# Optimization experiments

Measured on AMD Instinct MI355X. Metric: run time of the kernel, lower is better.

Reference implementation:

```python
import jax, jax.numpy as jnp
import numpy as np

B, T, D_MODEL = 2, 1024, 1024
H, DEPTH = 8, 5
DH = D_MODEL // H


def setup_inputs() -> dict:
    key = jax.random.key(0)
    k_x, k_wp, k_bp, k_wv, k_wo = jax.random.split(key, 5)
    x = jax.random.normal(k_x, (B, T, D_MODEL), dtype=jnp.float32)
    # Parameters stored as [in, out] (y = x @ W + b), equivalent math to nn.Linear.
    Wp = jax.random.normal(k_wp, (D_MODEL, H * DEPTH), dtype=jnp.float32) * 0.02
    bp = jnp.zeros((H * DEPTH,), dtype=jnp.float32)
    Wv = jax.random.normal(k_wv, (D_MODEL, D_MODEL), dtype=jnp.float32) * 0.02
    Wo = jax.random.normal(k_wo, (D_MODEL, D_MODEL), dtype=jnp.float32) * 0.02
    return {"x": x, "Wp": Wp, "bp": bp, "Wv": Wv, "Wo": Wo}


def reference(x, Wp, bp, Wv, Wo):
    Bx, Tx, d = x.shape
    # soft binary path decisions: B,H,T,DEPTH
    paths = jax.nn.sigmoid(x @ Wp + bp)              # B,T,H*DEPTH
    paths = paths.reshape(Bx, Tx, H, DEPTH).transpose(0, 2, 1, 3)  # B,H,T,DEPTH
    # pairwise per-level agreement: B,H,Tq,Tk,DEPTH
    pq = paths[:, :, :, None, :]
    pk = paths[:, :, None, :, :]
    agree = pq * pk + (1.0 - pq) * (1.0 - pk)
    # shared-prefix length via cumprod over depth, summed
    sim = jnp.cumprod(agree, axis=-1).sum(axis=-1) / DEPTH  # B,H,Tq,Tk
    # causal mask
    mask = jnp.triu(jnp.ones((Tx, Tx), dtype=bool), k=1)
    sim = jnp.where(mask[None, None], -jnp.inf, sim)
    attn = jax.nn.softmax(sim, axis=-1)              # B,H,T,T
    V = (x @ Wv).reshape(Bx, Tx, H, DH).transpose(0, 2, 1, 3)  # B,H,T,dh
    ctx = jnp.einsum('bhqk,bhkd->bhqd', attn, V)
    ctx = ctx.transpose(0, 2, 1, 3).reshape(Bx, Tx, d)
    return ctx @ Wo
```

## Files before the change

### kernel.cpp

```cpp
#include <hip/hip_runtime.h>
#include <hip/hip_bf16.h>

#define B_ 2
#define T_ 1024
#define D_ 1024
#define H_ 8
#define DEPTH_ 5
#define DH_ 128

typedef short s16x8 __attribute__((ext_vector_type(8)));
typedef short s16x4 __attribute__((ext_vector_type(4)));
typedef float f32x4 __attribute__((ext_vector_type(4)));

__device__ inline short f2bf(float f) {
  __hip_bfloat16 h = __float2bfloat16(f);
  return *reinterpret_cast<short*>(&h);
}

#define MFMA16(a, b, c) __builtin_amdgcn_mfma_f32_16x16x32_bf16(a, b, c, 0, 0, 0)

typedef __attribute__((address_space(3))) unsigned int lds_u32_t;
typedef __attribute__((address_space(1))) unsigned int glb_u32_t;
__device__ __forceinline__ void glds16(const void* g, void* l) {
  __builtin_amdgcn_global_load_lds((const glb_u32_t*)g, (lds_u32_t*)l, 16, 0,
                                   0);
}

__global__ __launch_bounds__(256) void prep_kernel(
    const float* __restrict__ Wv, const float* __restrict__ Wo,
    const float* __restrict__ Wp, const float* __restrict__ x,
    short* __restrict__ WBt, short* __restrict__ Wot,
    short* __restrict__ xb) {
  int tid = threadIdx.x;
  if (blockIdx.z < 2) {
    const float* W = blockIdx.z ? Wo : Wv;
    short* Wt = blockIdx.z ? Wot : WBt;
    __shared__ float tile[64][65];
    int k0 = blockIdx.y * 64, n0 = blockIdx.x * 64;
#pragma unroll
    for (int i = 0; i < 4; ++i) {
      int idx = tid + i * 256;
      int r = idx >> 4, c4 = (idx & 15) * 4;
      float4 v = *(const float4*)&W[(size_t)(k0 + r) * D_ + n0 + c4];
      tile[r][c4 + 0] = v.x;
      tile[r][c4 + 1] = v.y;
      tile[r][c4 + 2] = v.z;
      tile[r][c4 + 3] = v.w;
    }
    __syncthreads();
#pragma unroll
    for (int j = 0; j < 2; ++j) {
      int idx = tid + j * 256;
      int n = idx >> 3, k8 = (idx & 7) * 8;
      s16x8 outv;
#pragma unroll
      for (int jj = 0; jj < 8; ++jj) outv[jj] = f2bf(tile[k8 + jj][n]);
      *(s16x8*)&Wt[(size_t)(n0 + n) * D_ + k0 + k8] = outv;
    }
  } else {
    int bid = blockIdx.y * 16 + blockIdx.x;
#pragma unroll
    for (int c = 0; c < 4; ++c) {
      size_t idx = (size_t)bid * 8192 + c * 2048 + tid * 8;
      float4 f0 = *(const float4*)&x[idx];
      float4 f1 = *(const float4*)&x[idx + 4];
      s16x8 v;
      v[0] = f2bf(f0.x); v[1] = f2bf(f0.y);
      v[2] = f2bf(f0.z); v[3] = f2bf(f0.w);
      v[4] = f2bf(f1.x); v[5] = f2bf(f1.y);
      v[6] = f2bf(f1.z); v[7] = f2bf(f1.w);
      *(s16x8*)&xb[idx] = v;
    }
    if (bid < 4) {
#pragma unroll
      for (int it = 0; it < 8; ++it) {
        int item = bid * 2048 + it * 256 + tid;
        int row = item >> 7, k8 = (item & 127) * 8;
        s16x8 v;
        if (row < H_ * DEPTH_) {
#pragma unroll
          for (int j = 0; j < 8; ++j)
            v[j] = f2bf(Wp[(size_t)(k8 + j) * (H_ * DEPTH_) + row]);
        } else {
#pragma unroll
          for (int j = 0; j < 8; ++j) v[j] = 0;
        }
        *(s16x8*)&WBt[(size_t)(1024 + row) * D_ + k8] = v;
      }
    }
  }
}

template <int MODE>
__global__ __launch_bounds__(256) void gemm128(
    const short* __restrict__ A, const short* __restrict__ Bt,
    float* __restrict__ Cf, short* __restrict__ Vt,
    const float* __restrict__ bp, float* __restrict__ paths_t) {
  __shared__ short As[64 * 128];
  __shared__ short Bs[64 * 128];
  const int K = D_;
  int tid = threadIdx.x;
  int bm = blockIdx.y << 6, bn = blockIdx.x << 6;
  int w = tid >> 6, lane = tid & 63;
  int wm = (w >> 1) * 32, wn = (w & 1) * 32;
  int g = lane >> 4, fr = lane & 15;
  f32x4 acc[2][2] = {{{0.f, 0.f, 0.f, 0.f}, {0.f, 0.f, 0.f, 0.f}},
                     {{0.f, 0.f, 0.f, 0.f}, {0.f, 0.f, 0.f, 0.f}}};

  int r4 = lane >> 4;
  int cg = lane & 15;
  const short* Asrc[4];
  const short* Bsrc[4];
  short* Adst[4];
  short* Bdst[4];
#pragma unroll
  for (int i = 0; i < 4; ++i) {
    int row = w * 16 + i * 4 + r4;
    int scol = (cg ^ (row & 15)) * 8;
    Asrc[i] = A + (size_t)(bm + row) * K + scol;
    Bsrc[i] = Bt + (size_t)(bn + row) * K + scol;
    Adst[i] = &As[(w * 16 + i * 4) * 128];
    Bdst[i] = &Bs[(w * 16 + i * 4) * 128];
  }

  for (int k0 = 0; k0 < K; k0 += 128) {
    __syncthreads();
#pragma unroll
    for (int i = 0; i < 4; ++i) {
      glds16(Asrc[i] + k0, Adst[i]);
      glds16(Bsrc[i] + k0, Bdst[i]);
    }
    __syncthreads();
#pragma unroll
    for (int ks = 0; ks < 4; ++ks) {
      int p = ((ks * 4 + g) ^ fr) * 8;
      s16x8 a0 = *(const s16x8*)&As[(wm + fr) * 128 + p];
      s16x8 a1 = *(const s16x8*)&As[(wm + 16 + fr) * 128 + p];
      s16x8 b0 = *(const s16x8*)&Bs[(wn + fr) * 128 + p];
      s16x8 b1 = *(const s16x8*)&Bs[(wn + 16 + fr) * 128 + p];
      acc[0][0] = MFMA16(a0, b0, acc[0][0]);
      acc[0][1] = MFMA16(a0, b1, acc[0][1]);
      acc[1][0] = MFMA16(a1, b0, acc[1][0]);
      acc[1][1] = MFMA16(a1, b1, acc[1][1]);
    }
  }
  int col = lane & 15, rbase = (lane >> 4) * 4;
  if (MODE == 0) {
#pragma unroll
    for (int mi = 0; mi < 2; ++mi)
#pragma unroll
      for (int ni = 0; ni < 2; ++ni)
#pragma unroll
        for (int r = 0; r < 4; ++r)
          Cf[(size_t)(bm + wm + mi * 16 + rbase + r) * D_ + bn + wn +
             ni * 16 + col] = acc[mi][ni][r];
  } else if (bn < 1024) {
#pragma unroll
    for (int mi = 0; mi < 2; ++mi)
#pragma unroll
      for (int ni = 0; ni < 2; ++ni) {
        int m = bm + wm + mi * 16 + rbase;
        int n = bn + wn + ni * 16 + col;
        int b = m >> 10, t = m & (T_ - 1);
        int h = n >> 7, dh = n & (DH_ - 1);
        s16x4 v4;
#pragma unroll
        for (int r = 0; r < 4; ++r) v4[r] = f2bf(acc[mi][ni][r]);
        *(s16x4*)&Vt[((size_t)((b * H_ + h) * DH_ + dh)) * T_ + t] = v4;
      }
  } else {
#pragma unroll
    for (int ni = 0; ni < 2; ++ni) {
      int pn = wn + ni * 16 + col;
      if (pn < H_ * DEPTH_) {
        float bias = bp[pn];
        int h = pn / DEPTH_, d = pn % DEPTH_;
#pragma unroll
        for (int mi = 0; mi < 2; ++mi)
#pragma unroll
          for (int r = 0; r < 4; ++r) {
            int m = bm + wm + mi * 16 + rbase + r;
            int b = m >> 10, t = m & (T_ - 1);
            float pv = 1.f / (1.f + __expf(-(acc[mi][ni][r] + bias)));
            paths_t[(((size_t)(b * H_ + h) * T_ + t) * DEPTH_) + d] = pv;
          }
      }
    }
  }
}

#define LS2 136

__global__ __launch_bounds__(512) void attn_kernel(
    const float* __restrict__ paths_t, const short* __restrict__ Vt,
    short* __restrict__ ctxb) {
  int bh = blockIdx.y;
  int b = bh >> 3, h = bh & 7;
  int bx = blockIdx.x;
  int w = threadIdx.x >> 6, lane = threadIdx.x & 63;
  int g = lane >> 4, fr = lane & 15;

  __shared__ short Vs[DH_ * 128];
  __shared__ short Ss[32 * LS2];
  __shared__ float lsum_s[32];

  const float* pb = paths_t + (size_t)bh * T_ * DEPTH_;
  const short* vb = Vt + (size_t)bh * DH_ * T_;

  int r4 = lane >> 4, cg = lane & 15;
  const short* Vsrc[4];
  short* Vdst[4];
#pragma unroll
  for (int i = 0; i < 4; ++i) {
    int row = w * 16 + i * 4 + r4;
    int scol = (cg ^ (row & 15)) * 8;
    Vsrc[i] = vb + (size_t)row * T_ + scol;
    Vdst[i] = &Vs[(w * 16 + i * 4) * 128];
  }

  for (int half = 0; half < 2; ++half) {
    int qt = half ? (31 - bx) : bx;
    int q0 = qt * 32;
    int nkt = (qt >> 2) + 1;

    float pq[4][DEPTH_], mq[4][DEPTH_];
#pragma unroll
    for (int j = 0; j < 4; ++j) {
      const float* qr = pb + (size_t)(q0 + w * 4 + j) * DEPTH_;
#pragma unroll
      for (int d = 0; d < DEPTH_; ++d) {
        pq[j][d] = qr[d];
        mq[j][d] = 1.f - pq[j][d];
      }
    }
    f32x4 acc[2] = {{0.f, 0.f, 0.f, 0.f}, {0.f, 0.f, 0.f, 0.f}};
    float part[4] = {};

    for (int kt = 0; kt < nkt; ++kt) {
      int k0 = kt * 128;
      __syncthreads();
      int kA = k0 + lane, kB = k0 + 64 + lane;
      const float* krA = pb + (size_t)kA * DEPTH_;
      const float* krB = pb + (size_t)kB * DEPTH_;
      float pkA[DEPTH_], mkA[DEPTH_], pkB[DEPTH_], mkB[DEPTH_];
#pragma unroll
      for (int d = 0; d < DEPTH_; ++d) {
        pkA[d] = krA[d];
        pkB[d] = krB[d];
      }
#pragma unroll
      for (int i = 0; i < 4; ++i) glds16(Vsrc[i] + k0, Vdst[i]);
#pragma unroll
      for (int d = 0; d < DEPTH_; ++d) {
        mkA[d] = 1.f - pkA[d];
        mkB[d] = 1.f - pkB[d];
      }
#pragma unroll
      for (int j = 0; j < 4; ++j) {
        int qg = q0 + w * 4 + j;
        {
          float a0 = fmaf(pq[j][0], pkA[0], mq[j][0] * mkA[0]);
          float a1 = fmaf(pq[j][1], pkA[1], mq[j][1] * mkA[1]);
          float a2 = fmaf(pq[j][2], pkA[2], mq[j][2] * mkA[2]);
          float a3 = fmaf(pq[j][3], pkA[3], mq[j][3] * mkA[3]);
          float a4 = fmaf(pq[j][4], pkA[4], mq[j][4] * mkA[4]);
          float t4 = 1.f + a4;
          float t3 = fmaf(a3, t4, 1.f);
          float t2 = fmaf(a2, t3, 1.f);
          float t1 = fmaf(a1, t2, 1.f);
          float s = a0 * t1;
          float wv = (kA <= qg) ? __expf(s * 0.2f) : 0.f;
          part[j] += wv;
          Ss[(w * 4 + j) * LS2 + lane] = f2bf(wv);
        }
        {
          float a0 = fmaf(pq[j][0], pkB[0], mq[j][0] * mkB[0]);
          float a1 = fmaf(pq[j][1], pkB[1], mq[j][1] * mkB[1]);
          float a2 = fmaf(pq[j][2], pkB[2], mq[j][2] * mkB[2]);
          float a3 = fmaf(pq[j][3], pkB[3], mq[j][3] * mkB[3]);
          float a4 = fmaf(pq[j][4], pkB[4], mq[j][4] * mkB[4]);
          float t4 = 1.f + a4;
          float t3 = fmaf(a3, t4, 1.f);
          float t2 = fmaf(a2, t3, 1.f);
          float t1 = fmaf(a1, t2, 1.f);
          float s = a0 * t1;
          float wv = (kB <= qg) ? __expf(s * 0.2f) : 0.f;
          part[j] += wv;
          Ss[(w * 4 + j) * LS2 + 64 + lane] = f2bf(wv);
        }
      }
      __syncthreads();
#pragma unroll
      for (int ks = 0; ks < 4; ++ks) {
        int ko = ks * 32 + g * 8;
        int sl = ((ks * 4 + g) ^ fr) * 8;
        s16x8 sa0 = *(const s16x8*)&Ss[fr * LS2 + ko];
        s16x8 sa1 = *(const s16x8*)&Ss[(16 + fr) * LS2 + ko];
        s16x8 vv = *(const s16x8*)&Vs[(w * 16 + fr) * 128 + sl];
        acc[0] = MFMA16(sa0, vv, acc[0]);
        acc[1] = MFMA16(sa1, vv, acc[1]);
      }
    }
#pragma unroll
    for (int j = 0; j < 4; ++j) {
      float s = part[j];
#pragma unroll
      for (int off = 32; off >= 1; off >>= 1) s += __shfl_xor(s, off, 64);
      if (lane == j) lsum_s[w * 4 + j] = s;
    }
    __syncthreads();
    int col = fr, rbase = g * 4;
#pragma unroll
    for (int qt2 = 0; qt2 < 2; ++qt2)
#pragma unroll
      for (int r = 0; r < 4; ++r) {
        int ql = qt2 * 16 + rbase + r;
        int dh = w * 16 + col;
        float val = acc[qt2][r] / lsum_s[ql];
        ctxb[(size_t)(b * T_ + q0 + ql) * D_ + h * DH_ + dh] = f2bf(val);
      }
    __syncthreads();
  }
}

extern "C" void kernel_launch(void* const* d_in, const int* in_sizes, int n_in,
                              void* d_out, int out_size, void* d_ws,
                              size_t ws_size, hipStream_t stream) {
  const float* x = (const float*)d_in[0];
  const float* Wp = (const float*)d_in[1];
  const float* bp = (const float*)d_in[2];
  const float* Wv = (const float*)d_in[3];
  const float* Wo = (const float*)d_in[4];
  float* out = (float*)d_out;

  char* ws = (char*)d_ws;
  float* paths_t = (float*)ws;
  short* Vt = (short*)(ws + 327680);
  short* WBt = (short*)(ws + 4521984);
  short* Wot = (short*)(ws + 6750208);
  short* ctxb = (short*)(ws + 8847360);
  short* xb = (short*)(ws + 13041664);

  prep_kernel<<<dim3(16, 16, 3), 256, 0, stream>>>(Wv, Wo, Wp, x, WBt, Wot,
                                                   xb);
  gemm128<1><<<dim3(17, 32), 256, 0, stream>>>(xb, WBt, nullptr, Vt, bp,
                                               paths_t);
  attn_kernel<<<dim3(16, B_ * H_), 512, 0, stream>>>(paths_t, Vt, ctxb);
  gemm128<0><<<dim3(16, 32), 256, 0, stream>>>(ctxb, Wot, out, nullptr,
                                               nullptr, nullptr);
}
```

Baseline: 124.3 us.

## Double-buffer GEMM LDS tiles and enlarge block tile to 128x64

The bf16 GEMM kernel now uses two LDS buffers with K-tiles of 64, so the next tile's global-to-LDS loads are issued while the current tile is computed. Manual s_waitcnt and raw barriers replace the __syncthreads pairs. The block M tile doubles to 128 with 4x2 MFMA accumulators per wave, halving the grid. The aim is to hide load latency and raise data reuse, at the cost of fewer blocks, which is 272 or 256 on a large-CU GPU, and more registers.

New measurement: 132.2 us. +6.3%, slower.

```diff
diff --git a/kernel.cpp b/kernel.cpp
--- a/kernel.cpp
+++ b/kernel.cpp
@@ -25,6 +25,13 @@
   __builtin_amdgcn_global_load_lds((const glb_u32_t*)g, (lds_u32_t*)l, 16, 0,
                                    0);
 }
+
+#define BARRIER()                     \
+  {                                   \
+    asm volatile("" ::: "memory");    \
+    __builtin_amdgcn_s_barrier();     \
+    asm volatile("" ::: "memory");    \
+  }
 
 __global__ __launch_bounds__(256) void prep_kernel(
     const float* __restrict__ Wv, const float* __restrict__ Wo,
@@ -96,58 +103,87 @@
     const short* __restrict__ A, const short* __restrict__ Bt,
     float* __restrict__ Cf, short* __restrict__ Vt,
     const float* __restrict__ bp, float* __restrict__ paths_t) {
-  __shared__ short As[64 * 128];
-  __shared__ short Bs[64 * 128];
+  __shared__ short As[2][128 * 64];
+  __shared__ short Bs[2][64 * 64];
   const int K = D_;
   int tid = threadIdx.x;
-  int bm = blockIdx.y << 6, bn = blockIdx.x << 6;
+  int bm = blockIdx.y << 7, bn = blockIdx.x << 6;
   int w = tid >> 6, lane = tid & 63;
-  int wm = (w >> 1) * 32, wn = (w & 1) * 32;
+  int wm = (w >> 1) * 64, wn = (w & 1) * 32;
   int g = lane >> 4, fr = lane & 15;
-  f32x4 acc[2][2] = {{{0.f, 0.f, 0.f, 0.f}, {0.f, 0.f, 0.f, 0.f}},
-                     {{0.f, 0.f, 0.f, 0.f}, {0.f, 0.f, 0.f, 0.f}}};
-
-  int r4 = lane >> 4;
-  int cg = lane & 15;
+  f32x4 acc[4][2] = {};
+
+  int r8 = lane >> 3;
+  int scg = (lane & 7) ^ r8;
   const short* Asrc[4];
-  const short* Bsrc[4];
-  short* Adst[4];
-  short* Bdst[4];
-#pragma unroll
-  for (int i = 0; i < 4; ++i) {
-    int row = w * 16 + i * 4 + r4;
-    int scol = (cg ^ (row & 15)) * 8;
-    Asrc[i] = A + (size_t)(bm + row) * K + scol;
-    Bsrc[i] = Bt + (size_t)(bn + row) * K + scol;
-    Adst[i] = &As[(w * 16 + i * 4) * 128];
-    Bdst[i] = &Bs[(w * 16 + i * 4) * 128];
-  }
-
-  for (int k0 = 0; k0 < K; k0 += 128) {
-    __syncthreads();
-#pragma unroll
-    for (int i = 0; i < 4; ++i) {
-      glds16(Asrc[i] + k0, Adst[i]);
-      glds16(Bsrc[i] + k0, Bdst[i]);
-    }
-    __syncthreads();
-#pragma unroll
-    for (int ks = 0; ks < 4; ++ks) {
-      int p = ((ks * 4 + g) ^ fr) * 8;
-      s16x8 a0 = *(const s16x8*)&As[(wm + fr) * 128 + p];
-      s16x8 a1 = *(const s16x8*)&As[(wm + 16 + fr) * 128 + p];
-      s16x8 b0 = *(const s16x8*)&Bs[(wn + fr) * 128 + p];
-      s16x8 b1 = *(const s16x8*)&Bs[(wn + 16 + fr) * 128 + p];
-      acc[0][0] = MFMA16(a0, b0, acc[0][0]);
-      acc[0][1] = MFMA16(a0, b1, acc[0][1]);
-      acc[1][0] = MFMA16(a1, b0, acc[1][0]);
-      acc[1][1] = MFMA16(a1, b1, acc[1][1]);
-    }
-  }
+  const short* Bsrc[2];
+#pragma unroll
+  for (int i = 0; i < 4; ++i)
+    Asrc[i] = A + (size_t)(bm + w * 32 + i * 8 + r8) * K + scg * 8;
+#pragma unroll
+  for (int i = 0; i < 2; ++i)
+    Bsrc[i] = Bt + (size_t)(bn + w * 16 + i * 8 + r8) * K + scg * 8;
+
+#define STAGE(BUF, K0)                                    \
+  {                                                       \
+    glds16(Asrc[0] + (K0), &As[BUF][(w * 32 + 0) * 64]);  \
+    glds16(Asrc[1] + (K0), &As[BUF][(w * 32 + 8) * 64]);  \
+    glds16(Asrc[2] + (K0), &As[BUF][(w * 32 + 16) * 64]); \
+    glds16(Asrc[3] + (K0), &As[BUF][(w * 32 + 24) * 64]); \
+    glds16(Bsrc[0] + (K0), &Bs[BUF][(w * 16 + 0) * 64]);  \
+    glds16(Bsrc[1] + (K0), &Bs[BUF][(w * 16 + 8) * 64]);  \
+  }
+
+#define COMPUTE(BUF)                                                   \
+  {                                                                    \
+    _Pragma("unroll") for (int ks = 0; ks < 2; ++ks) {                 \
+      int slot = ((ks * 4 + g) ^ (fr & 7)) * 8;                        \
+      s16x8 a0 = *(const s16x8*)&As[BUF][(wm + fr) * 64 + slot];       \
+      s16x8 a1 = *(const s16x8*)&As[BUF][(wm + 16 + fr) * 64 + slot];  \
+      s16x8 a2 = *(const s16x8*)&As[BUF][(wm + 32 + fr) * 64 + slot];  \
+      s16x8 a3 = *(const s16x8*)&As[BUF][(wm + 48 + fr) * 64 + slot];  \
+      s16x8 b0 = *(const s16x8*)&Bs[BUF][(wn + fr) * 64 + slot];       \
+      s16x8 b1 = *(const s16x8*)&Bs[BUF][(wn + 16 + fr) * 64 + slot];  \
+      acc[0][0] = MFMA16(a0, b0, acc[0][0]);                           \
+      acc[0][1] = MFMA16(a0, b1, acc[0][1]);                           \
+      acc[1][0] = MFMA16(a1, b0, acc[1][0]);                           \
+      acc[1][1] = MFMA16(a1, b1, acc[1][1]);                           \
+      acc[2][0] = MFMA16(a2, b0, acc[2][0]);                           \
+      acc[2][1] = MFMA16(a2, b1, acc[2][1]);                           \
+      acc[3][0] = MFMA16(a3, b0, acc[3][0]);                           \
+      acc[3][1] = MFMA16(a3, b1, acc[3][1]);                           \
+    }                                                                  \
+  }
+
+  const int NKT = K / 64;
+  STAGE(0, 0);
+  for (int kt = 0; kt < NKT; kt += 2) {
+    BARRIER();
+    if (kt + 1 < NKT) {
+      STAGE(1, (kt + 1) * 64);
+      asm volatile("s_waitcnt vmcnt(6)" ::: "memory");
+    } else {
+      asm volatile("s_waitcnt vmcnt(0)" ::: "memory");
+    }
+    BARRIER();
+    COMPUTE(0);
+    BARRIER();
+    if (kt + 2 < NKT) {
+      STAGE(0, (kt + 2) * 64);
+      asm volatile("s_waitcnt vmcnt(6)" ::: "memory");
+    } else {
+      asm volatile("s_waitcnt vmcnt(0)" ::: "memory");
+    }
+    BARRIER();
+    COMPUTE(1);
+  }
+#undef STAGE
+#undef COMPUTE
+
   int col = lane & 15, rbase = (lane >> 4) * 4;
   if (MODE == 0) {
 #pragma unroll
-    for (int mi = 0; mi < 2; ++mi)
+    for (int mi = 0; mi < 4; ++mi)
 #pragma unroll
       for (int ni = 0; ni < 2; ++ni)
 #pragma unroll
@@ -156,7 +192,7 @@
              ni * 16 + col] = acc[mi][ni][r];
   } else if (bn < 1024) {
 #pragma unroll
-    for (int mi = 0; mi < 2; ++mi)
+    for (int mi = 0; mi < 4; ++mi)
 #pragma unroll
       for (int ni = 0; ni < 2; ++ni) {
         int m = bm + wm + mi * 16 + rbase;
@@ -176,7 +212,7 @@
         float bias = bp[pn];
         int h = pn / DEPTH_, d = pn % DEPTH_;
 #pragma unroll
-        for (int mi = 0; mi < 2; ++mi)
+        for (int mi = 0; mi < 4; ++mi)
 #pragma unroll
           for (int r = 0; r < 4; ++r) {
             int m = bm + wm + mi * 16 + rbase + r;
@@ -343,9 +379,9 @@
 
   prep_kernel<<<dim3(16, 16, 3), 256, 0, stream>>>(Wv, Wo, Wp, x, WBt, Wot,
                                                    xb);
-  gemm128<1><<<dim3(17, 32), 256, 0, stream>>>(xb, WBt, nullptr, Vt, bp,
+  gemm128<1><<<dim3(17, 16), 256, 0, stream>>>(xb, WBt, nullptr, Vt, bp,
                                                paths_t);
   attn_kernel<<<dim3(16, B_ * H_), 512, 0, stream>>>(paths_t, Vt, ctxb);
-  gemm128<0><<<dim3(16, 32), 256, 0, stream>>>(ctxb, Wot, out, nullptr,
+  gemm128<0><<<dim3(16, 16), 256, 0, stream>>>(ctxb, Wot, out, nullptr,
                                                nullptr, nullptr);
 }
```
